# Optimization experiments

Hardware: AMD Instinct MI355X
Metric: run time of the kernel (lower is better)

## Reference

```python
import jax, jax.numpy as jnp
import numpy as np
import math

B, IN, H = 4096, 1024, 1024

def setup_inputs() -> dict:
    key = jax.random.key(0)
    ks = jax.random.split(key, 20)
    stdv = 1.0 / math.sqrt(H)
    def U(k, shape):
        return jax.random.uniform(k, shape, jnp.float32, -stdv, stdv)
    inp = {
        'input_': jax.random.normal(ks[0], (B, IN), jnp.float32),
        'prev_h': jax.random.normal(ks[1], (B, H), jnp.float32),
        'prev_c': jax.random.normal(ks[2], (B, H), jnp.float32),
    }
    names = ['ii', 'hi', 'if_', 'hf', 'ig', 'hg', 'io', 'ho']
    for n, kw, kb in zip(names, ks[3:11], ks[11:19]):
        in_dim = IN if n[0] == 'i' else H
        inp['W_' + n] = U(kw, (H, in_dim))  # torch Linear weight is (out, in)
        inp['b_' + n] = U(kb, (H,))
    return inp

def reference(input_, prev_h, prev_c,
              W_ii, b_ii, W_hi, b_hi, W_if_, b_if_, W_hf, b_hf,
              W_ig, b_ig, W_hg, b_hg, W_io, b_io, W_ho, b_ho):
    # Fuse the 8 small GEMMs into 2 batched GEMMs over stacked gate weights.
    Wx = jnp.concatenate([W_ii, W_if_, W_ig, W_io], axis=0)   # (4H, IN)
    Wh = jnp.concatenate([W_hi, W_hf, W_hg, W_ho], axis=0)    # (4H, H)
    bx = jnp.concatenate([b_ii, b_if_, b_ig, b_io], axis=0)   # (4H,)
    bh = jnp.concatenate([b_hi, b_hf, b_hg, b_ho], axis=0)
    gates = input_ @ Wx.T + prev_h @ Wh.T + bx + bh           # (B, 4H)
    i, f, g, o = jnp.split(gates, 4, axis=-1)
    i = jax.nn.sigmoid(i)
    f = jax.nn.sigmoid(f)
    g = jnp.tanh(g)
    o = jax.nn.sigmoid(o)
    c = f * prev_c + i * g
    h = o * jnp.tanh(c)
    return (h, c)
```

## Files before the change

### kernel.cpp

```cpp
#include <hip/hip_runtime.h>
#include <hip/hip_bf16.h>
#include <stdint.h>


#define BDIM 4096
#define HDIM 1024
#define KDIM 2048
#define BK   64
#define NT   (KDIM / BK)

typedef __attribute__((ext_vector_type(8))) short bf16x8;
typedef __attribute__((ext_vector_type(4))) float f32x4;
typedef __attribute__((ext_vector_type(8))) unsigned short u16x8;

__device__ __forceinline__ unsigned short f2bf(float f) {
  union { float f; uint32_t u; } v; v.f = f;
  uint32_t u = v.u;
  u += 0x7FFFu + ((u >> 16) & 1);
  return (unsigned short)(u >> 16);
}


__global__ __launch_bounds__(256) void pack_A_kernel(const float* __restrict__ x,
                                                     const float* __restrict__ h,
                                                     unsigned short* __restrict__ Ap) {
  int t = blockIdx.x * 256 + threadIdx.x;
  int b = t >> 8;
  int k = (t & 255) << 3;
  const float* src = (k < 1024) ? (x + (size_t)b * 1024 + k)
                                : (h + (size_t)b * 1024 + (k - 1024));
  float4 v0 = *(const float4*)src;
  float4 v1 = *(const float4*)(src + 4);
  u16x8 o;
  o[0] = f2bf(v0.x); o[1] = f2bf(v0.y); o[2] = f2bf(v0.z); o[3] = f2bf(v0.w);
  o[4] = f2bf(v1.x); o[5] = f2bf(v1.y); o[6] = f2bf(v1.z); o[7] = f2bf(v1.w);
  *(u16x8*)(Ap + (size_t)b * 2048 + k) = o;
}

__global__ __launch_bounds__(256) void pack_W_kernel(
    const float* __restrict__ W_ii, const float* __restrict__ W_if,
    const float* __restrict__ W_ig, const float* __restrict__ W_io,
    const float* __restrict__ W_hi, const float* __restrict__ W_hf,
    const float* __restrict__ W_hg, const float* __restrict__ W_ho,
    unsigned short* __restrict__ Wp) {
  int t = blockIdx.x * 256 + threadIdx.x;
  int r = t >> 8;
  int k = (t & 255) << 3;
  int g = r >> 10;
  int u = r & 1023;
  const float* wx = (g == 0) ? W_ii : (g == 1) ? W_if : (g == 2) ? W_ig : W_io;
  const float* wh = (g == 0) ? W_hi : (g == 1) ? W_hf : (g == 2) ? W_hg : W_ho;
  const float* src = (k < 1024) ? (wx + (size_t)u * 1024 + k)
                                : (wh + (size_t)u * 1024 + (k - 1024));
  float4 v0 = *(const float4*)src;
  float4 v1 = *(const float4*)(src + 4);
  u16x8 o;
  o[0] = f2bf(v0.x); o[1] = f2bf(v0.y); o[2] = f2bf(v0.z); o[3] = f2bf(v0.w);
  o[4] = f2bf(v1.x); o[5] = f2bf(v1.y); o[6] = f2bf(v1.z); o[7] = f2bf(v1.w);
  *(u16x8*)(Wp + (size_t)r * 2048 + k) = o;
}


#define GLOAD_LDS16(g, l)                                                            \
  __builtin_amdgcn_global_load_lds(                                                  \
      (const __attribute__((address_space(1))) unsigned int*)(g),                    \
      (__attribute__((address_space(3))) unsigned int*)(l), 16, 0, 0)

__device__ __forceinline__ float fast_sigmoid(float x) {
  return 1.f / (1.f + __expf(-x));
}
__device__ __forceinline__ float fast_tanh(float x) {
  return 1.f - 2.f / (1.f + __expf(2.f * x));
}

__global__ __launch_bounds__(256) void lstm_gemm_kernel(
    const unsigned short* __restrict__ Ap, const unsigned short* __restrict__ Wp,
    const float* __restrict__ b_ii, const float* __restrict__ b_hi,
    const float* __restrict__ b_if, const float* __restrict__ b_hf,
    const float* __restrict__ b_ig, const float* __restrict__ b_hg,
    const float* __restrict__ b_io, const float* __restrict__ b_ho,
    const float* __restrict__ prev_c,
    float* __restrict__ out_h, float* __restrict__ out_c) {
  __shared__ unsigned short As[128][64];
  __shared__ unsigned short Ws[128][64];

  const int tid  = threadIdx.x;
  const int lane = tid & 63;
  const int wave = tid >> 6;
  const int mblk = blockIdx.x;
  const int ublk = blockIdx.y;
  const int wm   = wave >> 1;
  const int wu   = wave & 1;

  f32x4 acc[4][4];
#pragma unroll
  for (int g = 0; g < 4; ++g)
#pragma unroll
    for (int m = 0; m < 4; ++m) acc[g][m] = (f32x4){0.f, 0.f, 0.f, 0.f};

  const int rsub = lane >> 3;
  const int csub = (lane & 7) << 3;
  const unsigned short* ga0 = Ap + (size_t)(mblk * 128 + wave * 32 + rsub) * 2048 + csub;
  const unsigned short* gw0 = Wp + (size_t)(wave * 1024 + ublk * 32 + rsub) * 2048 + csub;

  for (int kt = 0; kt < NT; ++kt) {
    const unsigned short* ga = ga0 + kt * BK;
    const unsigned short* gw = gw0 + kt * BK;
#pragma unroll
    for (int j = 0; j < 4; ++j) {
      GLOAD_LDS16(ga + (size_t)j * 8 * 2048, &As[wave * 32 + j * 8][0]);
      GLOAD_LDS16(gw + (size_t)j * 8 * 2048, &Ws[wave * 32 + j * 8][0]);
    }
    __syncthreads();

#pragma unroll
    for (int kk = 0; kk < 2; ++kk) {
      const int kb = kk * 32 + ((lane >> 4) << 3);
      bf16x8 af[4], bfr[4];
#pragma unroll
      for (int m = 0; m < 4; ++m)
        af[m] = *(const bf16x8*)&As[wm * 64 + m * 16 + (lane & 15)][kb];
#pragma unroll
      for (int g = 0; g < 4; ++g)
        bfr[g] = *(const bf16x8*)&Ws[g * 32 + wu * 16 + (lane & 15)][kb];
#pragma unroll
      for (int g = 0; g < 4; ++g)
#pragma unroll
        for (int m = 0; m < 4; ++m)
          acc[g][m] = __builtin_amdgcn_mfma_f32_16x16x32_bf16(af[m], bfr[g], acc[g][m], 0, 0, 0);
    }
    __syncthreads();
  }

  const int u = ublk * 32 + wu * 16 + (lane & 15);
  const float bs_i = b_ii[u] + b_hi[u];
  const float bs_f = b_if[u] + b_hf[u];
  const float bs_g = b_ig[u] + b_hg[u];
  const float bs_o = b_io[u] + b_ho[u];

#pragma unroll
  for (int m = 0; m < 4; ++m) {
    const int rbase = mblk * 128 + wm * 64 + m * 16 + ((lane >> 4) << 2);
#pragma unroll
    for (int r = 0; r < 4; ++r) {
      const int row = rbase + r;
      const float gi = fast_sigmoid(acc[0][m][r] + bs_i);
      const float gf = fast_sigmoid(acc[1][m][r] + bs_f);
      const float gg = fast_tanh   (acc[2][m][r] + bs_g);
      const float go = fast_sigmoid(acc[3][m][r] + bs_o);
      const float cp = prev_c[(size_t)row * 1024 + u];
      const float c  = gf * cp + gi * gg;
      const float hh = go * fast_tanh(c);
      out_h[(size_t)row * 1024 + u] = hh;
      out_c[(size_t)row * 1024 + u] = c;
    }
  }
}


extern "C" void kernel_launch(void* const* d_in, const int* in_sizes, int n_in,
                              void* d_out, int out_size, void* d_ws, size_t ws_size,
                              hipStream_t stream) {
  const float* input_ = (const float*)d_in[0];
  const float* prev_h = (const float*)d_in[1];
  const float* prev_c = (const float*)d_in[2];
  const float* W_ii = (const float*)d_in[3];  const float* b_ii = (const float*)d_in[4];
  const float* W_hi = (const float*)d_in[5];  const float* b_hi = (const float*)d_in[6];
  const float* W_if = (const float*)d_in[7];  const float* b_if = (const float*)d_in[8];
  const float* W_hf = (const float*)d_in[9];  const float* b_hf = (const float*)d_in[10];
  const float* W_ig = (const float*)d_in[11]; const float* b_ig = (const float*)d_in[12];
  const float* W_hg = (const float*)d_in[13]; const float* b_hg = (const float*)d_in[14];
  const float* W_io = (const float*)d_in[15]; const float* b_io = (const float*)d_in[16];
  const float* W_ho = (const float*)d_in[17]; const float* b_ho = (const float*)d_in[18];

  unsigned short* Ap = (unsigned short*)d_ws;
  unsigned short* Wp = Ap + (size_t)4096 * 2048;

  pack_A_kernel<<<4096, 256, 0, stream>>>(input_, prev_h, Ap);
  pack_W_kernel<<<4096, 256, 0, stream>>>(W_ii, W_if, W_ig, W_io,
                                          W_hi, W_hf, W_hg, W_ho, Wp);

  float* out_h = (float*)d_out;
  float* out_c = out_h + (size_t)4096 * 1024;
  dim3 grid(32, 32);
  lstm_gemm_kernel<<<grid, 256, 0, stream>>>(Ap, Wp,
                                             b_ii, b_hi, b_if, b_hf,
                                             b_ig, b_hg, b_io, b_ho,
                                             prev_c, out_h, out_c);
}
```

Measured before the change: 252.0 us.

## Rewrite LSTM GEMM with 256x256 tiles, double-buffered LDS pipeline, and merged pack kernel

Replaces the 128x128-tile, single-buffered GEMM with a 512-thread kernel that computes 256x256 output tiles. It double-buffers 128 KB of XOR-swizzled LDS, staging loads with global_load_lds under explicit waitcnt and barrier scheduling, and raises MFMA priority with setprio. The weight packing is reordered so each 64-row group interleaves the four gates, and both pack kernels are merged into one launch. The block index is remapped for locality. The aim is to cut global traffic, hide load latency, and avoid LDS bank conflicts, at the cost of heavy register and LDS use and fragile hand-scheduled synchronisation.

New measurement: 213.2 us. 1.18x faster.

```diff
diff --git a/kernel.cpp b/kernel.cpp
--- a/kernel.cpp
+++ b/kernel.cpp
@@ -2,12 +2,6 @@
 #include <hip/hip_bf16.h>
 #include <stdint.h>
 
-
-#define BDIM 4096
-#define HDIM 1024
-#define KDIM 2048
-#define BK   64
-#define NT   (KDIM / BK)
 
 typedef __attribute__((ext_vector_type(8))) short bf16x8;
 typedef __attribute__((ext_vector_type(4))) float f32x4;
@@ -19,61 +13,88 @@
   u += 0x7FFFu + ((u >> 16) & 1);
   return (unsigned short)(u >> 16);
 }
-
-
-__global__ __launch_bounds__(256) void pack_A_kernel(const float* __restrict__ x,
-                                                     const float* __restrict__ h,
-                                                     unsigned short* __restrict__ Ap) {
-  int t = blockIdx.x * 256 + threadIdx.x;
-  int b = t >> 8;
-  int k = (t & 255) << 3;
-  const float* src = (k < 1024) ? (x + (size_t)b * 1024 + k)
-                                : (h + (size_t)b * 1024 + (k - 1024));
+__device__ __forceinline__ float fast_sigmoid(float x) { return 1.f / (1.f + __expf(-x)); }
+__device__ __forceinline__ float fast_tanh(float x) { return 1.f - 2.f / (1.f + __expf(2.f * x)); }
+
+__global__ __launch_bounds__(256) void pack_kernel(
+    const float* __restrict__ x, const float* __restrict__ hprev,
+    const float* __restrict__ W_ii, const float* __restrict__ W_if,
+    const float* __restrict__ W_ig, const float* __restrict__ W_io,
+    const float* __restrict__ W_hi, const float* __restrict__ W_hf,
+    const float* __restrict__ W_hg, const float* __restrict__ W_ho,
+    unsigned short* __restrict__ Ap, unsigned short* __restrict__ Wp) {
+  const int bid = blockIdx.x;
+  const int k = threadIdx.x << 3;
+  const float* src;
+  unsigned short* dst;
+  if (bid < 4096) {
+    const int b = bid;
+    src = (k < 1024) ? (x + (size_t)b * 1024 + k) : (hprev + (size_t)b * 1024 + (k - 1024));
+    dst = Ap + (size_t)b * 2048 + k;
+  } else {
+    const int rp = bid - 4096;
+    const int g = (rp >> 4) & 3;
+    const int u = ((rp >> 6) << 4) | (rp & 15);
+    const float* wx = (g == 0) ? W_ii : (g == 1) ? W_if : (g == 2) ? W_ig : W_io;
+    const float* wh = (g == 0) ? W_hi : (g == 1) ? W_hf : (g == 2) ? W_hg : W_ho;
+    src = (k < 1024) ? (wx + (size_t)u * 1024 + k) : (wh + (size_t)u * 1024 + (k - 1024));
+    dst = Wp + (size_t)rp * 2048 + k;
+  }
   float4 v0 = *(const float4*)src;
   float4 v1 = *(const float4*)(src + 4);
   u16x8 o;
   o[0] = f2bf(v0.x); o[1] = f2bf(v0.y); o[2] = f2bf(v0.z); o[3] = f2bf(v0.w);
   o[4] = f2bf(v1.x); o[5] = f2bf(v1.y); o[6] = f2bf(v1.z); o[7] = f2bf(v1.w);
-  *(u16x8*)(Ap + (size_t)b * 2048 + k) = o;
-}
-
-__global__ __launch_bounds__(256) void pack_W_kernel(
-    const float* __restrict__ W_ii, const float* __restrict__ W_if,
-    const float* __restrict__ W_ig, const float* __restrict__ W_io,
-    const float* __restrict__ W_hi, const float* __restrict__ W_hf,
-    const float* __restrict__ W_hg, const float* __restrict__ W_ho,
-    unsigned short* __restrict__ Wp) {
-  int t = blockIdx.x * 256 + threadIdx.x;
-  int r = t >> 8;
-  int k = (t & 255) << 3;
-  int g = r >> 10;
-  int u = r & 1023;
-  const float* wx = (g == 0) ? W_ii : (g == 1) ? W_if : (g == 2) ? W_ig : W_io;
-  const float* wh = (g == 0) ? W_hi : (g == 1) ? W_hf : (g == 2) ? W_hg : W_ho;
-  const float* src = (k < 1024) ? (wx + (size_t)u * 1024 + k)
-                                : (wh + (size_t)u * 1024 + (k - 1024));
-  float4 v0 = *(const float4*)src;
-  float4 v1 = *(const float4*)(src + 4);
-  u16x8 o;
-  o[0] = f2bf(v0.x); o[1] = f2bf(v0.y); o[2] = f2bf(v0.z); o[3] = f2bf(v0.w);
-  o[4] = f2bf(v1.x); o[5] = f2bf(v1.y); o[6] = f2bf(v1.z); o[7] = f2bf(v1.w);
-  *(u16x8*)(Wp + (size_t)r * 2048 + k) = o;
-}
-
-
-#define GLOAD_LDS16(g, l)                                                            \
+  *(u16x8*)dst = o;
+}
+
+
+#define GL16(g, l)                                                                   \
   __builtin_amdgcn_global_load_lds(                                                  \
       (const __attribute__((address_space(1))) unsigned int*)(g),                    \
       (__attribute__((address_space(3))) unsigned int*)(l), 16, 0, 0)
 
-__device__ __forceinline__ float fast_sigmoid(float x) {
-  return 1.f / (1.f + __expf(-x));
-}
-__device__ __forceinline__ float fast_tanh(float x) {
-  return 1.f - 2.f / (1.f + __expf(2.f * x));
-}
-
-__global__ __launch_bounds__(256) void lstm_gemm_kernel(
+#define STAGE_A(BUF, H, KT)                                                          \
+  { GL16(pA0 + (size_t)(H) * 524288 + (size_t)(KT) * 128,                            \
+         lds + (BUF) * 32768 + (H) * 16384 + wvoff);                                 \
+    GL16(pA1 + (size_t)(H) * 524288 + (size_t)(KT) * 128,                            \
+         lds + (BUF) * 32768 + (H) * 16384 + 8192 + wvoff); }
+#define STAGE_B(BUF, H, KT)                                                          \
+  { GL16(pB0 + (size_t)(H) * 524288 + (size_t)(KT) * 128,                            \
+         lds + 65536 + (BUF) * 32768 + (H) * 16384 + wvoff);                         \
+    GL16(pB1 + (size_t)(H) * 524288 + (size_t)(KT) * 128,                            \
+         lds + 65536 + (BUF) * 32768 + (H) * 16384 + 8192 + wvoff); }
+
+#define DS_A(BUF, QQ)                                                                \
+  { const char* Ab_ = lds + (BUF) * 32768 + tbA + (QQ) * 4096;                       \
+    a00 = *(const bf16x8*)(Ab_);        a01 = *(const bf16x8*)(Ab_ + 64);            \
+    a10 = *(const bf16x8*)(Ab_ + 2048); a11 = *(const bf16x8*)(Ab_ + 2048 + 64); }
+
+#define DS_B(BUF)                                                                    \
+  { const char* Bb_ = lds + 65536 + (BUF) * 32768 + tbB;                             \
+    _Pragma("unroll")                                                                \
+    for (int ni = 0; ni < 4; ++ni) {                                                 \
+      breg[ni][0] = *(const bf16x8*)(Bb_ + ni * 2048);                               \
+      breg[ni][1] = *(const bf16x8*)(Bb_ + ni * 2048 + 64);                          \
+    } }
+
+#define MFMA_CLUSTER(QQ)                                                             \
+  { __builtin_amdgcn_s_setprio(1);                                                   \
+    _Pragma("unroll")                                                                \
+    for (int ni = 0; ni < 4; ++ni) {                                                 \
+      acc[2*(QQ)][ni]   = __builtin_amdgcn_mfma_f32_16x16x32_bf16(a00, breg[ni][0], acc[2*(QQ)][ni], 0,0,0);   \
+      acc[2*(QQ)][ni]   = __builtin_amdgcn_mfma_f32_16x16x32_bf16(a01, breg[ni][1], acc[2*(QQ)][ni], 0,0,0);   \
+      acc[2*(QQ)+1][ni] = __builtin_amdgcn_mfma_f32_16x16x32_bf16(a10, breg[ni][0], acc[2*(QQ)+1][ni], 0,0,0); \
+      acc[2*(QQ)+1][ni] = __builtin_amdgcn_mfma_f32_16x16x32_bf16(a11, breg[ni][1], acc[2*(QQ)+1][ni], 0,0,0); \
+    }                                                                                \
+    __builtin_amdgcn_s_setprio(0); }
+
+#define BAR()      __builtin_amdgcn_s_barrier()
+#define LGKM0()    asm volatile("s_waitcnt lgkmcnt(0)" ::: "memory")
+#define LGKM8()    asm volatile("s_waitcnt lgkmcnt(8)" ::: "memory")
+#define VMC4()     asm volatile("s_waitcnt vmcnt(4)" ::: "memory")
+
+__global__ __launch_bounds__(512, 2) void lstm_gemm_kernel(
     const unsigned short* __restrict__ Ap, const unsigned short* __restrict__ Wp,
     const float* __restrict__ b_ii, const float* __restrict__ b_hi,
     const float* __restrict__ b_if, const float* __restrict__ b_hf,
@@ -81,73 +102,118 @@
     const float* __restrict__ b_io, const float* __restrict__ b_ho,
     const float* __restrict__ prev_c,
     float* __restrict__ out_h, float* __restrict__ out_c) {
-  __shared__ unsigned short As[128][64];
-  __shared__ unsigned short Ws[128][64];
+  __shared__ char lds[131072];
 
   const int tid  = threadIdx.x;
   const int lane = tid & 63;
-  const int wave = tid >> 6;
-  const int mblk = blockIdx.x;
-  const int ublk = blockIdx.y;
-  const int wm   = wave >> 1;
-  const int wu   = wave & 1;
-
-  f32x4 acc[4][4];
-#pragma unroll
-  for (int g = 0; g < 4; ++g)
-#pragma unroll
-    for (int m = 0; m < 4; ++m) acc[g][m] = (f32x4){0.f, 0.f, 0.f, 0.f};
-
-  const int rsub = lane >> 3;
-  const int csub = (lane & 7) << 3;
-  const unsigned short* ga0 = Ap + (size_t)(mblk * 128 + wave * 32 + rsub) * 2048 + csub;
-  const unsigned short* gw0 = Wp + (size_t)(wave * 1024 + ublk * 32 + rsub) * 2048 + csub;
-
-  for (int kt = 0; kt < NT; ++kt) {
-    const unsigned short* ga = ga0 + kt * BK;
-    const unsigned short* gw = gw0 + kt * BK;
-#pragma unroll
-    for (int j = 0; j < 4; ++j) {
-      GLOAD_LDS16(ga + (size_t)j * 8 * 2048, &As[wave * 32 + j * 8][0]);
-      GLOAD_LDS16(gw + (size_t)j * 8 * 2048, &Ws[wave * 32 + j * 8][0]);
-    }
-    __syncthreads();
-
-#pragma unroll
-    for (int kk = 0; kk < 2; ++kk) {
-      const int kb = kk * 32 + ((lane >> 4) << 3);
-      bf16x8 af[4], bfr[4];
-#pragma unroll
-      for (int m = 0; m < 4; ++m)
-        af[m] = *(const bf16x8*)&As[wm * 64 + m * 16 + (lane & 15)][kb];
-#pragma unroll
-      for (int g = 0; g < 4; ++g)
-        bfr[g] = *(const bf16x8*)&Ws[g * 32 + wu * 16 + (lane & 15)][kb];
-#pragma unroll
-      for (int g = 0; g < 4; ++g)
-#pragma unroll
-        for (int m = 0; m < 4; ++m)
-          acc[g][m] = __builtin_amdgcn_mfma_f32_16x16x32_bf16(af[m], bfr[g], acc[g][m], 0, 0, 0);
-    }
-    __syncthreads();
+  const int wv   = tid >> 6;
+  const int wm   = wv >> 2;
+  const int wn   = wv & 3;
+
+  const int bid = blockIdx.x;
+  const int sid = (bid & 7) * 32 + (bid >> 3);
+  const int bx  = sid & 15;
+  const int by  = sid >> 4;
+
+  const int r0  = tid >> 3;
+  const int r1  = (tid + 512) >> 3;
+  const int kb0 = ((tid & 7) << 4) ^ (((r0 >> 2) & 1) << 5);
+  const int kb1 = ((tid & 7) << 4) ^ (((r1 >> 2) & 1) << 5);
+  const char* ApC = (const char*)Ap;
+  const char* BpC = (const char*)Wp;
+  const char* pA0 = ApC + (size_t)(bx * 256 + r0) * 4096 + kb0;
+  const char* pA1 = ApC + (size_t)(bx * 256 + r1) * 4096 + kb1;
+  const char* pB0 = BpC + (size_t)(by * 256 + r0) * 4096 + kb0;
+  const char* pB1 = BpC + (size_t)(by * 256 + r1) * 4096 + kb1;
+  const int wvoff = wv * 1024;
+
+  const int qeff16 = (((lane >> 4) ^ (((lane >> 2) & 1) << 1)) << 4);
+  const int tbA = (wm * 128 + (lane & 15)) * 128 + qeff16;
+  const int tbB = (wn * 64 + (lane & 15)) * 128 + qeff16;
+
+  f32x4 acc[8][4];
+#pragma unroll
+  for (int mi = 0; mi < 8; ++mi)
+#pragma unroll
+    for (int ni = 0; ni < 4; ++ni) acc[mi][ni] = (f32x4){0.f, 0.f, 0.f, 0.f};
+
+  bf16x8 breg[4][2];
+  bf16x8 a00, a01, a10, a11;
+
+  STAGE_B(0, 0, 0); STAGE_B(0, 1, 0);
+  STAGE_A(0, 0, 0); STAGE_A(0, 1, 0);
+  STAGE_B(1, 0, 1); STAGE_B(1, 1, 1);
+  VMC4();
+  BAR();
+
+  for (int i = 0; i < 16; ++i) {
+    const int T  = i << 1;
+    const int k1 = (T + 1) & 31;
+    const int k2 = (T + 2) & 31;
+    const int k3 = (T + 3) & 31;
+
+    DS_B(0); DS_A(0, 0);
+    STAGE_A(1, 0, k1);
+    LGKM8();
+    BAR(); LGKM0();
+    MFMA_CLUSTER(0);
+    BAR();
+    DS_A(0, 1);
+    STAGE_A(1, 1, k1);
+    BAR(); LGKM0();
+    MFMA_CLUSTER(1);
+    BAR();
+    DS_A(0, 2);
+    STAGE_B(0, 0, k2);
+    BAR(); LGKM0();
+    MFMA_CLUSTER(2);
+    BAR();
+    DS_A(0, 3);
+    STAGE_B(0, 1, k2);
+    VMC4();
+    BAR(); LGKM0();
+    MFMA_CLUSTER(3);
+    BAR();
+    DS_B(1); DS_A(1, 0);
+    STAGE_A(0, 0, k2);
+    LGKM8();
+    BAR(); LGKM0();
+    MFMA_CLUSTER(0);
+    BAR();
+    DS_A(1, 1);
+    STAGE_A(0, 1, k2);
+    BAR(); LGKM0();
+    MFMA_CLUSTER(1);
+    BAR();
+    DS_A(1, 2);
+    STAGE_B(1, 0, k3);
+    BAR(); LGKM0();
+    MFMA_CLUSTER(2);
+    BAR();
+    DS_A(1, 3);
+    STAGE_B(1, 1, k3);
+    VMC4();
+    BAR(); LGKM0();
+    MFMA_CLUSTER(3);
+    BAR();
   }
 
-  const int u = ublk * 32 + wu * 16 + (lane & 15);
-  const float bs_i = b_ii[u] + b_hi[u];
-  const float bs_f = b_if[u] + b_hf[u];
-  const float bs_g = b_ig[u] + b_hg[u];
-  const float bs_o = b_io[u] + b_ho[u];
-
-#pragma unroll
-  for (int m = 0; m < 4; ++m) {
-    const int rbase = mblk * 128 + wm * 64 + m * 16 + ((lane >> 4) << 2);
-#pragma unroll
-    for (int r = 0; r < 4; ++r) {
-      const int row = rbase + r;
-      const float gi = fast_sigmoid(acc[0][m][r] + bs_i);
-      const float gf = fast_sigmoid(acc[1][m][r] + bs_f);
-      const float gg = fast_tanh   (acc[2][m][r] + bs_g);
-      const float go = fast_sigmoid(acc[3][m][r] + bs_o);
+  const int u = ((by * 4 + wn) << 4) + (lane & 15);
+  const float bsum0 = b_ii[u] + b_hi[u];
+  const float bsum1 = b_if[u] + b_hf[u];
+  const float bsum2 = b_ig[u] + b_hg[u];
+  const float bsum3 = b_io[u] + b_ho[u];
+  const int row0 = bx * 256 + wm * 128 + ((lane >> 4) << 2);
+
+#pragma unroll
+  for (int mi = 0; mi < 8; ++mi) {
+#pragma unroll
+    for (int rr = 0; rr < 4; ++rr) {
+      const int row = row0 + mi * 16 + rr;
+      const float gi = fast_sigmoid(acc[mi][0][rr] + bsum0);
+      const float gf = fast_sigmoid(acc[mi][1][rr] + bsum1);
+      const float gg = fast_tanh   (acc[mi][2][rr] + bsum2);
+      const float go = fast_sigmoid(acc[mi][3][rr] + bsum3);
       const float cp = prev_c[(size_t)row * 1024 + u];
       const float c  = gf * cp + gi * gg;
       const float hh = go * fast_tanh(c);
@@ -176,15 +242,14 @@
   unsigned short* Ap = (unsigned short*)d_ws;
   unsigned short* Wp = Ap + (size_t)4096 * 2048;
 
-  pack_A_kernel<<<4096, 256, 0, stream>>>(input_, prev_h, Ap);
-  pack_W_kernel<<<4096, 256, 0, stream>>>(W_ii, W_if, W_ig, W_io,
-                                          W_hi, W_hf, W_hg, W_ho, Wp);
+  pack_kernel<<<8192, 256, 0, stream>>>(input_, prev_h,
+                                        W_ii, W_if, W_ig, W_io,
+                                        W_hi, W_hf, W_hg, W_ho, Ap, Wp);
 
   float* out_h = (float*)d_out;
   float* out_c = out_h + (size_t)4096 * 1024;
-  dim3 grid(32, 32);
-  lstm_gemm_kernel<<<grid, 256, 0, stream>>>(Ap, Wp,
-                                             b_ii, b_hi, b_if, b_hf,
-                                             b_ig, b_hg, b_io, b_ho,
-                                             prev_c, out_h, out_c);
-}
+  lstm_gemm_kernel<<<256, 512, 0, stream>>>(Ap, Wp,
+                                            b_ii, b_hi, b_if, b_hf,
+                                            b_ig, b_hg, b_io, b_ho,
+                                            prev_c, out_h, out_c);
+}
```
